# Performance work log

Measured on AMD Instinct MI355X. Metric: run time of the kernel, lower is better.

## Reference

```python
import jax, jax.numpy as jnp
import numpy as np

NUM_NODES = 65536      # 16 graphs x 4096 nodes
NODES_PER_GRAPH = 4096
NUM_GRAPHS = 16
NUM_EDGES = 1048576    # avg degree 16
DIM = 64


def setup_inputs() -> dict:
    key = jax.random.key(0)
    ks = jax.random.split(key, 10)
    # edges constrained within each component graph (batched-graph semantics)
    eper = NUM_EDGES // NUM_GRAPHS
    gid = np.repeat(np.arange(NUM_GRAPHS), eper)
    rng = np.random.default_rng(0)
    src = jnp.asarray(rng.integers(0, NODES_PER_GRAPH, NUM_EDGES) + gid * NODES_PER_GRAPH, dtype=jnp.int64)
    dst = jnp.asarray(rng.integers(0, NODES_PER_GRAPH, NUM_EDGES) + gid * NODES_PER_GRAPH, dtype=jnp.int64)
    s = 1.0 / np.sqrt(DIM)
    return {
        "x": jax.random.normal(ks[0], (NUM_NODES, DIM), dtype=jnp.float32),
        "W1": jax.random.normal(ks[1], (DIM, DIM), dtype=jnp.float32) * s,
        "b1": jnp.zeros((DIM,), dtype=jnp.float32),
        "W2": jax.random.normal(ks[2], (DIM, DIM), dtype=jnp.float32) * s,
        "b2": jnp.zeros((DIM,), dtype=jnp.float32),
        "W3": jax.random.normal(ks[3], (DIM, DIM), dtype=jnp.float32) * s,
        "b3": jnp.zeros((DIM,), dtype=jnp.float32),
        "src": src,
        "dst": dst,
        "num_graphs": NUM_GRAPHS,
    }


def _sym_norms(src, dst, n):
    ones = jnp.ones(src.shape[0], dtype=jnp.float32)
    deg_out = jax.ops.segment_sum(ones, src, num_segments=n)
    deg_in = jax.ops.segment_sum(ones, dst, num_segments=n)
    inv_sqrt = lambda d: jnp.where(d > 0, d, 1.0) ** -0.5 * (d > 0)
    return inv_sqrt(deg_out), inv_sqrt(deg_in)


def _graph_conv(x, W, b, src, dst, norm_src, norm_dst, n):
    # DGL GraphConv, norm='both': h = D_in^{-1/2} A D_out^{-1/2} (X W) + b
    h = (x * norm_src[:, None]) @ W          # [N, D]
    msg = h[src]                              # [E, D] gather
    agg = jax.ops.segment_sum(msg, dst, num_segments=n)  # [N, D] scatter-add
    return agg * norm_dst[:, None] + b


def reference(x, W1, b1, W2, b2, W3, b3, src, dst, num_graphs):
    n = x.shape[0]
    norm_src, norm_dst = _sym_norms(src, dst, n)
    h = _graph_conv(x, W1, b1, src, dst, norm_src, norm_dst, n)
    h = _graph_conv(h, W2, b2, src, dst, norm_src, norm_dst, n)
    h = _graph_conv(h, W3, b3, src, dst, norm_src, norm_dst, n)
    # unbatch + pad to max_num_nodes + stack; equal-size graphs -> pure reshape
    return h.reshape(num_graphs, n // num_graphs, h.shape[-1])
```

## Files before the change

kernel.cpp:

```cpp
#include <hip/hip_runtime.h>
#include <hip/hip_fp16.h>

#define DIM 64
#define NG  16
#define CPG 16
#define NPG 4096
#define LSTR 68
#define HISTB (NG*CPG)
#define GGN 32

__global__ __launch_bounds__(256) void k1_hist_gemm(
    const int* __restrict__ src, const int* __restrict__ dst,
    int* __restrict__ hsub, int* __restrict__ dsub, int chunk, int npg,
    const float* __restrict__ x, const float* __restrict__ W1,
    __half* __restrict__ hout, int swiz)
{
    __shared__ int smem[8192];
    const int tid = threadIdx.x;
    if ((int)blockIdx.x < HISTB) {
        int* hs = smem;
        int* hd = smem + NPG;
        const int blk = blockIdx.x;
        const int g = blk / CPG;
        const int ebase = blk * chunk;
        const int nbase = g * npg;
        for (int i = tid; i < npg; i += 256) { hs[i] = 0; hd[i] = 0; }
        __syncthreads();
        for (int e = tid; e < chunk; e += 256) {
            atomicAdd(&hs[src[ebase + e] - nbase], 1);
            atomicAdd(&hd[dst[ebase + e] - nbase], 1);
        }
        __syncthreads();
        for (int i = tid; i < npg; i += 256) {
            hsub[blk * npg + i] = hs[i];
            dsub[blk * npg + i] = hd[i];
        }
    } else {
        float* Wt = (float*)smem;
        float* xs = Wt + 64 * LSTR;
        int blk = blockIdx.x - HISTB;
        if (swiz) {
            int xg = blk & 7;
            int j = blk >> 3;
            int g = xg + ((j >> 7) << 3);
            blk = (g << 7) + (j & 127);
        }
        const int row0 = blk * 32;
        for (int i = tid; i < 64 * 64; i += 256) {
            int k = i >> 6, c = i & 63;
            Wt[c * LSTR + k] = W1[i];
        }
        for (int i = tid; i < 32 * 64; i += 256) {
            int r = i >> 6, c = i & 63;
            xs[r * LSTR + c] = x[(size_t)(row0 + r) * 64 + c];
        }
        __syncthreads();
        const int c0 = tid & 31;
        const int r0 = tid >> 5;
        float acc[4][2] = {};
#pragma unroll
        for (int k = 0; k < 64; k += 4) {
            float4 w0 = *(const float4*)&Wt[(c0     ) * LSTR + k];
            float4 w1 = *(const float4*)&Wt[(c0 + 32) * LSTR + k];
#pragma unroll
            for (int rr = 0; rr < 4; ++rr) {
                float4 xv = *(const float4*)&xs[(r0 + 8 * rr) * LSTR + k];
                acc[rr][0] += xv.x * w0.x + xv.y * w0.y + xv.z * w0.z + xv.w * w0.w;
                acc[rr][1] += xv.x * w1.x + xv.y * w1.y + xv.z * w1.z + xv.w * w1.w;
            }
        }
#pragma unroll
        for (int rr = 0; rr < 4; ++rr) {
            int row = row0 + r0 + 8 * rr;
            hout[(size_t)row * 64 + c0     ] = __float2half_rn(acc[rr][0]);
            hout[(size_t)row * 64 + c0 + 32] = __float2half_rn(acc[rr][1]);
        }
    }
}

__global__ __launch_bounds__(1024) void k2_scan(
    const int* __restrict__ hsub, int* __restrict__ dsub,
    float* __restrict__ ns, float* __restrict__ nd,
    int* __restrict__ rowptr, int epg, int npg, int N, int E)
{
    __shared__ int ddeg[NPG];
    __shared__ int wsum[16];
    const int g = blockIdx.x;
    const int t = threadIdx.x;
    const int nbase = g * npg;
    const int ebase = g * epg;
    for (int i = t; i < npg; i += 1024) {
        int sd = 0, dd = 0;
#pragma unroll
        for (int k = 0; k < CPG; ++k) {
            sd += hsub[(g * CPG + k) * npg + i];
            dd += dsub[(g * CPG + k) * npg + i];
        }
        ns[nbase + i] = sd > 0 ? rsqrtf((float)sd) : 0.0f;
        nd[nbase + i] = dd > 0 ? rsqrtf((float)dd) : 0.0f;
        ddeg[i] = dd;
    }
    __syncthreads();
    const int i0 = 4 * t;
    int d0 = ddeg[i0], d1 = ddeg[i0 + 1], d2 = ddeg[i0 + 2], d3 = ddeg[i0 + 3];
    int s4 = d0 + d1 + d2 + d3;
    const int lane = t & 63, wid = t >> 6;
    int v = s4;
#pragma unroll
    for (int off = 1; off < 64; off <<= 1) {
        int u = __shfl_up(v, off, 64);
        if (lane >= off) v += u;
    }
    if (lane == 63) wsum[wid] = v;
    __syncthreads();
    if (t < 16) {
        int w = wsum[t];
#pragma unroll
        for (int off = 1; off < 16; off <<= 1) {
            int u = __shfl_up(w, off, 16);
            if (t >= off) w += u;
        }
        wsum[t] = w;
    }
    __syncthreads();
    int incl = v + (wid > 0 ? wsum[wid - 1] : 0);
    int c = ebase + incl - s4;
    rowptr[nbase + i0    ] = c; ddeg[i0    ] = c; c += d0;
    rowptr[nbase + i0 + 1] = c; ddeg[i0 + 1] = c; c += d1;
    rowptr[nbase + i0 + 2] = c; ddeg[i0 + 2] = c; c += d2;
    rowptr[nbase + i0 + 3] = c; ddeg[i0 + 3] = c;
    if (g == 0 && t == 0) rowptr[N] = E;
    __syncthreads();
    for (int i = t; i < npg; i += 1024) {
        int cc = ddeg[i];
#pragma unroll
        for (int k = 0; k < CPG; ++k) {
            int* p = &dsub[(g * CPG + k) * npg + i];
            int old = *p; *p = cc; cc += old;
        }
    }
}

__global__ __launch_bounds__(256) void k3_fill(
    const int* __restrict__ src, const int* __restrict__ dst,
    const int* __restrict__ dsub, int* __restrict__ ssrc, int chunk, int npg)
{
    __shared__ int cur[NPG];
    const int blk = blockIdx.x;
    const int g = blk / CPG;
    const int t = threadIdx.x;
    const int ebase = blk * chunk;
    const int nbase = g * npg;
    for (int i = t; i < npg; i += 256) cur[i] = dsub[blk * npg + i];
    __syncthreads();
    for (int e = t; e < chunk; e += 256) {
        int s = src[ebase + e];
        int d = dst[ebase + e] - nbase;
        int pos = atomicAdd(&cur[d], 1);
        ssrc[pos] = s;
    }
}

__device__ __forceinline__ void acc_h4(float4& acc, uint2 u)
{
    __half2 p = *(__half2*)&u.x;
    __half2 q = *(__half2*)&u.y;
    float2 f0 = __half22float2(p);
    float2 f1 = __half22float2(q);
    acc.x += f0.x; acc.y += f0.y; acc.z += f1.x; acc.w += f1.y;
}

__device__ __forceinline__ void acc_h4s(float4& acc, uint2 u, float s)
{
    __half2 p = *(__half2*)&u.x;
    __half2 q = *(__half2*)&u.y;
    float2 f0 = __half22float2(p);
    float2 f1 = __half22float2(q);
    acc.x += s * f0.x; acc.y += s * f0.y; acc.z += s * f1.x; acc.w += s * f1.y;
}

__device__ __forceinline__ float4 gather_node(
    const __half* __restrict__ h, const int* __restrict__ ssrc,
    const float* __restrict__ ns, int beg, int end, int sub, int nsfold)
{
    float4 acc = {0.f, 0.f, 0.f, 0.f};
    int j = beg;
    if (nsfold) {
        for (; j + 7 < end; j += 8) {
            int s0 = ssrc[j+0], s1 = ssrc[j+1], s2 = ssrc[j+2], s3 = ssrc[j+3];
            int s4 = ssrc[j+4], s5 = ssrc[j+5], s6 = ssrc[j+6], s7 = ssrc[j+7];
            float n0 = ns[s0], n1 = ns[s1], n2 = ns[s2], n3 = ns[s3];
            float n4 = ns[s4], n5 = ns[s5], n6 = ns[s6], n7 = ns[s7];
            uint2 u0 = *(const uint2*)(h + (size_t)s0 * 64 + sub * 4);
            uint2 u1 = *(const uint2*)(h + (size_t)s1 * 64 + sub * 4);
            uint2 u2 = *(const uint2*)(h + (size_t)s2 * 64 + sub * 4);
            uint2 u3 = *(const uint2*)(h + (size_t)s3 * 64 + sub * 4);
            uint2 u4 = *(const uint2*)(h + (size_t)s4 * 64 + sub * 4);
            uint2 u5 = *(const uint2*)(h + (size_t)s5 * 64 + sub * 4);
            uint2 u6 = *(const uint2*)(h + (size_t)s6 * 64 + sub * 4);
            uint2 u7 = *(const uint2*)(h + (size_t)s7 * 64 + sub * 4);
            acc_h4s(acc, u0, n0); acc_h4s(acc, u1, n1);
            acc_h4s(acc, u2, n2); acc_h4s(acc, u3, n3);
            acc_h4s(acc, u4, n4); acc_h4s(acc, u5, n5);
            acc_h4s(acc, u6, n6); acc_h4s(acc, u7, n7);
        }
    } else {
        for (; j + 7 < end; j += 8) {
            int s0 = ssrc[j+0], s1 = ssrc[j+1], s2 = ssrc[j+2], s3 = ssrc[j+3];
            int s4 = ssrc[j+4], s5 = ssrc[j+5], s6 = ssrc[j+6], s7 = ssrc[j+7];
            uint2 u0 = *(const uint2*)(h + (size_t)s0 * 64 + sub * 4);
            uint2 u1 = *(const uint2*)(h + (size_t)s1 * 64 + sub * 4);
            uint2 u2 = *(const uint2*)(h + (size_t)s2 * 64 + sub * 4);
            uint2 u3 = *(const uint2*)(h + (size_t)s3 * 64 + sub * 4);
            uint2 u4 = *(const uint2*)(h + (size_t)s4 * 64 + sub * 4);
            uint2 u5 = *(const uint2*)(h + (size_t)s5 * 64 + sub * 4);
            uint2 u6 = *(const uint2*)(h + (size_t)s6 * 64 + sub * 4);
            uint2 u7 = *(const uint2*)(h + (size_t)s7 * 64 + sub * 4);
            acc_h4(acc, u0); acc_h4(acc, u1); acc_h4(acc, u2); acc_h4(acc, u3);
            acc_h4(acc, u4); acc_h4(acc, u5); acc_h4(acc, u6); acc_h4(acc, u7);
        }
    }
    int rem = end - j;
    if (rem > 0) {
#pragma unroll
        for (int q = 0; q < 4; ++q) {
            int jj = j + (q < rem ? q : rem - 1);
            int s = ssrc[jj];
            uint2 u = *(const uint2*)(h + (size_t)s * 64 + sub * 4);
            float sc = (q < rem) ? (nsfold ? ns[s] : 1.0f) : 0.0f;
            acc_h4s(acc, u, sc);
        }
    }
    if (rem > 4) {
#pragma unroll
        for (int q = 4; q < 8; ++q) {
            int jj = j + (q < rem ? q : rem - 1);
            int s = ssrc[jj];
            uint2 u = *(const uint2*)(h + (size_t)s * 64 + sub * 4);
            float sc = (q < rem) ? (nsfold ? ns[s] : 1.0f) : 0.0f;
            acc_h4s(acc, u, sc);
        }
    }
    return acc;
}

__global__ __launch_bounds__(256) void gg_kernel(
    const __half* __restrict__ h, const int* __restrict__ ssrc,
    const int* __restrict__ rowptr, const float* __restrict__ ns,
    const float* __restrict__ nd, const float* __restrict__ bprev,
    const float* __restrict__ W, __half* __restrict__ hout,
    int N, int nsfold, int swiz)
{
    __shared__ float Ws[64 * 64];
    __shared__ float us[GGN][64];
    int blk = blockIdx.x;
    if (swiz) {
        int xg = blk & 7;
        int j = blk >> 3;
        int g = xg + ((j >> 7) << 3);
        blk = (g << 7) + (j & 127);
    }
    const int tid = threadIdx.x;
    for (int i = tid; i < 64 * 64; i += 256) Ws[i] = W[i];

    const int wv = tid >> 6;
    const int lane = tid & 63;
    const int grp = lane >> 4;
    const int sub = lane & 15;

#pragma unroll
    for (int p = 0; p < GGN / 16; ++p) {
        int nl = p * 16 + wv * 4 + grp;
        int w = blk * GGN + nl;
        if (w < N) {
            int beg = rowptr[w], end = rowptr[w + 1];
            float4 acc = gather_node(h, ssrc, ns, beg, end, sub, nsfold);
            float sw = ns[w];
            float alpha = nd[w] * sw;
            float4 bv = *(const float4*)(bprev + sub * 4);
            float4 uo;
            uo.x = acc.x * alpha + sw * bv.x;
            uo.y = acc.y * alpha + sw * bv.y;
            uo.z = acc.z * alpha + sw * bv.z;
            uo.w = acc.w * alpha + sw * bv.w;
            *(float4*)&us[nl][sub * 4] = uo;
        }
    }
    __syncthreads();
    const int c = tid & 63;
#pragma unroll
    for (int m = 0; m < 8; ++m) {
        int nl = (tid >> 6) + 4 * m;
        int w = blk * GGN + nl;
        if (w >= N) continue;
        const float* ur = us[nl];
        float y = 0.f;
#pragma unroll
        for (int k = 0; k < 64; k += 4) {
            float4 uv = *(const float4*)&ur[k];
            y += uv.x * Ws[(k    ) * 64 + c]
               + uv.y * Ws[(k + 1) * 64 + c]
               + uv.z * Ws[(k + 2) * 64 + c]
               + uv.w * Ws[(k + 3) * 64 + c];
        }
        hout[(size_t)w * 64 + c] = __float2half_rn(y);
    }
}

__global__ __launch_bounds__(256) void gather_kernel(
    const __half* __restrict__ h, const int* __restrict__ ssrc,
    const int* __restrict__ rowptr, float* __restrict__ out,
    const float* __restrict__ nd, const float* __restrict__ b,
    int N, int swiz)
{
    int blk = blockIdx.x;
    if (swiz) {
        int x = blk & 7;
        int j = blk >> 3;
        int g = x + ((j >> 8) << 3);
        blk = (g << 8) + (j & 255);
    }
    const int wv = threadIdx.x >> 6;
    const int lane = threadIdx.x & 63;
    const int grp = lane >> 4;
    const int sub = lane & 15;
    int w = blk * 16 + wv * 4 + grp;
    if (w >= N) return;
    int beg = rowptr[w], end = rowptr[w + 1];
    float4 acc = gather_node(h, ssrc, (const float*)nullptr, beg, end, sub, 0);
    float n = nd[w];
    const float4 bv = *(const float4*)(b + sub * 4);
    acc.x = acc.x * n + bv.x;
    acc.y = acc.y * n + bv.y;
    acc.z = acc.z * n + bv.z;
    acc.w = acc.w * n + bv.w;
    *(float4*)(out + (size_t)w * 64 + sub * 4) = acc;
}

extern "C" void kernel_launch(void* const* d_in, const int* in_sizes, int n_in,
                              void* d_out, int out_size, void* d_ws, size_t ws_size,
                              hipStream_t stream)
{
    const float* x  = (const float*)d_in[0];
    const float* W1 = (const float*)d_in[1];
    const float* b1 = (const float*)d_in[2];
    const float* W2 = (const float*)d_in[3];
    const float* b2 = (const float*)d_in[4];
    const float* W3 = (const float*)d_in[5];
    const float* b3 = (const float*)d_in[6];
    const int*  src = (const int*)d_in[7];
    const int*  dst = (const int*)d_in[8];

    const int E = in_sizes[7];
    const int N = in_sizes[0] / DIM;
    const int epg = E / NG;
    const int npg = N / NG;
    const int chunk = epg / CPG;

    float*  ns     = (float*)d_ws;
    float*  nd     = ns + N;
    __half* hA     = (__half*)(nd + N);
    __half* hB     = hA + (size_t)N * DIM;
    int*    rowptr = (int*)(hB + (size_t)N * DIM);
    int*    ssrc   = rowptr + N + 1;
    int*    hsub   = ssrc + E;
    int*    dsub   = hsub + (size_t)HISTB * npg;
    float*  agg    = (float*)d_out;

    const int swiz = (N == 65536 && npg == 4096) ? 1 : 0;

    k1_hist_gemm<<<HISTB + N / 32, 256, 0, stream>>>(
        src, dst, hsub, dsub, chunk, npg, x, W1, hA, swiz);
    k2_scan<<<NG, 1024, 0, stream>>>(
        hsub, dsub, ns, nd, rowptr, epg, npg, N, E);
    k3_fill<<<HISTB, 256, 0, stream>>>(src, dst, dsub, ssrc, chunk, npg);

    gg_kernel<<<N / GGN, 256, 0, stream>>>(
        hA, ssrc, rowptr, ns, nd, b1, W2, hB, N, 1, swiz);
    gg_kernel<<<N / GGN, 256, 0, stream>>>(
        hB, ssrc, rowptr, ns, nd, b2, W3, hA, N, 0, swiz);
    gather_kernel<<<N / 16, 256, 0, stream>>>(
        hA, ssrc, rowptr, agg, nd, b3, N, swiz);
}
```

Baseline: 237.2 us.

## Prescale first-layer features by source norm and widen gathers to 16-byte loads

The first GEMM now writes fp32 output, and extra blocks in the CSR fill kernel scale it by the source-degree norm and convert it to fp16. This removes the per-edge ns[] lookups from the first gather layer. The gather path now uses 8 lanes per node with uint4 loads and software-pipelined index/feature prefetch, so each block handles twice as many nodes. gg_kernel drops the shared-memory copy of W, reads W from global/L1 with register blocking over 8 rows, and adds an occupancy hint to launch_bounds. The cost is an extra fp32 buffer write and read, plus higher register pressure.

```diff
diff --git a/kernel.cpp b/kernel.cpp
--- a/kernel.cpp
+++ b/kernel.cpp
@@ -8,12 +8,13 @@
 #define LSTR 68
 #define HISTB (NG*CPG)
 #define GGN 32
+#define USTR 68
 
 __global__ __launch_bounds__(256) void k1_hist_gemm(
     const int* __restrict__ src, const int* __restrict__ dst,
     int* __restrict__ hsub, int* __restrict__ dsub, int chunk, int npg,
     const float* __restrict__ x, const float* __restrict__ W1,
-    __half* __restrict__ hout, int swiz)
+    float* __restrict__ hout, int swiz)
 {
     __shared__ int smem[8192];
     const int tid = threadIdx.x;
@@ -72,8 +73,8 @@
 #pragma unroll
         for (int rr = 0; rr < 4; ++rr) {
             int row = row0 + r0 + 8 * rr;
-            hout[(size_t)row * 64 + c0     ] = __float2half_rn(acc[rr][0]);
-            hout[(size_t)row * 64 + c0 + 32] = __float2half_rn(acc[rr][1]);
+            hout[(size_t)row * 64 + c0     ] = acc[rr][0];
+            hout[(size_t)row * 64 + c0 + 32] = acc[rr][1];
         }
     }
 }
@@ -143,82 +144,113 @@
 
 __global__ __launch_bounds__(256) void k3_fill(
     const int* __restrict__ src, const int* __restrict__ dst,
-    const int* __restrict__ dsub, int* __restrict__ ssrc, int chunk, int npg)
-{
-    __shared__ int cur[NPG];
-    const int blk = blockIdx.x;
-    const int g = blk / CPG;
+    const int* __restrict__ dsub, int* __restrict__ ssrc, int chunk, int npg,
+    const float* __restrict__ hA32, const float* __restrict__ ns,
+    __half* __restrict__ hF)
+{
     const int t = threadIdx.x;
-    const int ebase = blk * chunk;
-    const int nbase = g * npg;
-    for (int i = t; i < npg; i += 256) cur[i] = dsub[blk * npg + i];
-    __syncthreads();
-    for (int e = t; e < chunk; e += 256) {
-        int s = src[ebase + e];
-        int d = dst[ebase + e] - nbase;
-        int pos = atomicAdd(&cur[d], 1);
-        ssrc[pos] = s;
-    }
-}
-
-__device__ __forceinline__ void acc_h4(float4& acc, uint2 u)
-{
-    __half2 p = *(__half2*)&u.x;
-    __half2 q = *(__half2*)&u.y;
-    float2 f0 = __half22float2(p);
-    float2 f1 = __half22float2(q);
-    acc.x += f0.x; acc.y += f0.y; acc.z += f1.x; acc.w += f1.y;
-}
-
-__device__ __forceinline__ void acc_h4s(float4& acc, uint2 u, float s)
-{
-    __half2 p = *(__half2*)&u.x;
-    __half2 q = *(__half2*)&u.y;
-    float2 f0 = __half22float2(p);
-    float2 f1 = __half22float2(q);
-    acc.x += s * f0.x; acc.y += s * f0.y; acc.z += s * f1.x; acc.w += s * f1.y;
-}
-
-__device__ __forceinline__ float4 gather_node(
+    if ((int)blockIdx.x < HISTB) {
+        __shared__ int cur[NPG];
+        const int blk = blockIdx.x;
+        const int g = blk / CPG;
+        const int ebase = blk * chunk;
+        const int nbase = g * npg;
+        for (int i = t; i < npg; i += 256) cur[i] = dsub[blk * npg + i];
+        __syncthreads();
+        for (int e = t; e < chunk; e += 256) {
+            int s = src[ebase + e];
+            int d = dst[ebase + e] - nbase;
+            int pos = atomicAdd(&cur[d], 1);
+            ssrc[pos] = s;
+        }
+    } else {
+        const int sb = blockIdx.x - HISTB;
+        const int base = sb * 16384;
+#pragma unroll
+        for (int it = 0; it < 16; ++it) {
+            int pos = base + it * 1024 + t * 4;
+            float4 v = *(const float4*)(hA32 + pos);
+            float s = ns[pos >> 6];
+            __half2 p0 = __floats2half2_rn(v.x * s, v.y * s);
+            __half2 p1 = __floats2half2_rn(v.z * s, v.w * s);
+            uint2 o;
+            o.x = *(const unsigned int*)&p0;
+            o.y = *(const unsigned int*)&p1;
+            *(uint2*)(hF + pos) = o;
+        }
+    }
+}
+
+__device__ __forceinline__ void acc_u4(float4& A, float4& B, uint4 u)
+{
+    __half2 h0 = *(__half2*)&u.x;
+    __half2 h1 = *(__half2*)&u.y;
+    __half2 h2 = *(__half2*)&u.z;
+    __half2 h3 = *(__half2*)&u.w;
+    float2 f0 = __half22float2(h0), f1 = __half22float2(h1);
+    float2 f2 = __half22float2(h2), f3 = __half22float2(h3);
+    A.x += f0.x; A.y += f0.y; A.z += f1.x; A.w += f1.y;
+    B.x += f2.x; B.y += f2.y; B.z += f3.x; B.w += f3.y;
+}
+
+__device__ __forceinline__ void acc_u4s(float4& A, float4& B, uint4 u, float s)
+{
+    __half2 h0 = *(__half2*)&u.x;
+    __half2 h1 = *(__half2*)&u.y;
+    __half2 h2 = *(__half2*)&u.z;
+    __half2 h3 = *(__half2*)&u.w;
+    float2 f0 = __half22float2(h0), f1 = __half22float2(h1);
+    float2 f2 = __half22float2(h2), f3 = __half22float2(h3);
+    A.x += s * f0.x; A.y += s * f0.y; A.z += s * f1.x; A.w += s * f1.y;
+    B.x += s * f2.x; B.y += s * f2.y; B.z += s * f3.x; B.w += s * f3.y;
+}
+
+__device__ __forceinline__ void gather_node8(
     const __half* __restrict__ h, const int* __restrict__ ssrc,
-    const float* __restrict__ ns, int beg, int end, int sub, int nsfold)
-{
-    float4 acc = {0.f, 0.f, 0.f, 0.f};
+    int beg, int end, int sub, float4& A, float4& B)
+{
+    const size_t off = (size_t)sub * 8;
     int j = beg;
-    if (nsfold) {
-        for (; j + 7 < end; j += 8) {
-            int s0 = ssrc[j+0], s1 = ssrc[j+1], s2 = ssrc[j+2], s3 = ssrc[j+3];
-            int s4 = ssrc[j+4], s5 = ssrc[j+5], s6 = ssrc[j+6], s7 = ssrc[j+7];
-            float n0 = ns[s0], n1 = ns[s1], n2 = ns[s2], n3 = ns[s3];
-            float n4 = ns[s4], n5 = ns[s5], n6 = ns[s6], n7 = ns[s7];
-            uint2 u0 = *(const uint2*)(h + (size_t)s0 * 64 + sub * 4);
-            uint2 u1 = *(const uint2*)(h + (size_t)s1 * 64 + sub * 4);
-            uint2 u2 = *(const uint2*)(h + (size_t)s2 * 64 + sub * 4);
-            uint2 u3 = *(const uint2*)(h + (size_t)s3 * 64 + sub * 4);
-            uint2 u4 = *(const uint2*)(h + (size_t)s4 * 64 + sub * 4);
-            uint2 u5 = *(const uint2*)(h + (size_t)s5 * 64 + sub * 4);
-            uint2 u6 = *(const uint2*)(h + (size_t)s6 * 64 + sub * 4);
-            uint2 u7 = *(const uint2*)(h + (size_t)s7 * 64 + sub * 4);
-            acc_h4s(acc, u0, n0); acc_h4s(acc, u1, n1);
-            acc_h4s(acc, u2, n2); acc_h4s(acc, u3, n3);
-            acc_h4s(acc, u4, n4); acc_h4s(acc, u5, n5);
-            acc_h4s(acc, u6, n6); acc_h4s(acc, u7, n7);
-        }
-    } else {
-        for (; j + 7 < end; j += 8) {
-            int s0 = ssrc[j+0], s1 = ssrc[j+1], s2 = ssrc[j+2], s3 = ssrc[j+3];
-            int s4 = ssrc[j+4], s5 = ssrc[j+5], s6 = ssrc[j+6], s7 = ssrc[j+7];
-            uint2 u0 = *(const uint2*)(h + (size_t)s0 * 64 + sub * 4);
-            uint2 u1 = *(const uint2*)(h + (size_t)s1 * 64 + sub * 4);
-            uint2 u2 = *(const uint2*)(h + (size_t)s2 * 64 + sub * 4);
-            uint2 u3 = *(const uint2*)(h + (size_t)s3 * 64 + sub * 4);
-            uint2 u4 = *(const uint2*)(h + (size_t)s4 * 64 + sub * 4);
-            uint2 u5 = *(const uint2*)(h + (size_t)s5 * 64 + sub * 4);
-            uint2 u6 = *(const uint2*)(h + (size_t)s6 * 64 + sub * 4);
-            uint2 u7 = *(const uint2*)(h + (size_t)s7 * 64 + sub * 4);
-            acc_h4(acc, u0); acc_h4(acc, u1); acc_h4(acc, u2); acc_h4(acc, u3);
-            acc_h4(acc, u4); acc_h4(acc, u5); acc_h4(acc, u6); acc_h4(acc, u7);
-        }
+    const int last = end - 8;
+    if (j <= last) {
+        int s0 = ssrc[j+0], s1 = ssrc[j+1], s2 = ssrc[j+2], s3 = ssrc[j+3];
+        int s4 = ssrc[j+4], s5 = ssrc[j+5], s6 = ssrc[j+6], s7 = ssrc[j+7];
+        uint4 a0 = *(const uint4*)(h + (size_t)s0 * 64 + off);
+        uint4 a1 = *(const uint4*)(h + (size_t)s1 * 64 + off);
+        uint4 a2 = *(const uint4*)(h + (size_t)s2 * 64 + off);
+        uint4 a3 = *(const uint4*)(h + (size_t)s3 * 64 + off);
+        uint4 a4 = *(const uint4*)(h + (size_t)s4 * 64 + off);
+        uint4 a5 = *(const uint4*)(h + (size_t)s5 * 64 + off);
+        uint4 a6 = *(const uint4*)(h + (size_t)s6 * 64 + off);
+        uint4 a7 = *(const uint4*)(h + (size_t)s7 * 64 + off);
+        j += 8;
+        bool more = (j <= last);
+        if (more) {
+            s0 = ssrc[j+0]; s1 = ssrc[j+1]; s2 = ssrc[j+2]; s3 = ssrc[j+3];
+            s4 = ssrc[j+4]; s5 = ssrc[j+5]; s6 = ssrc[j+6]; s7 = ssrc[j+7];
+        }
+        while (more) {
+            uint4 b0 = *(const uint4*)(h + (size_t)s0 * 64 + off);
+            uint4 b1 = *(const uint4*)(h + (size_t)s1 * 64 + off);
+            uint4 b2 = *(const uint4*)(h + (size_t)s2 * 64 + off);
+            uint4 b3 = *(const uint4*)(h + (size_t)s3 * 64 + off);
+            uint4 b4 = *(const uint4*)(h + (size_t)s4 * 64 + off);
+            uint4 b5 = *(const uint4*)(h + (size_t)s5 * 64 + off);
+            uint4 b6 = *(const uint4*)(h + (size_t)s6 * 64 + off);
+            uint4 b7 = *(const uint4*)(h + (size_t)s7 * 64 + off);
+            j += 8;
+            more = (j <= last);
+            if (more) {
+                s0 = ssrc[j+0]; s1 = ssrc[j+1]; s2 = ssrc[j+2]; s3 = ssrc[j+3];
+                s4 = ssrc[j+4]; s5 = ssrc[j+5]; s6 = ssrc[j+6]; s7 = ssrc[j+7];
+            }
+            acc_u4(A, B, a0); acc_u4(A, B, a1); acc_u4(A, B, a2); acc_u4(A, B, a3);
+            acc_u4(A, B, a4); acc_u4(A, B, a5); acc_u4(A, B, a6); acc_u4(A, B, a7);
+            a0 = b0; a1 = b1; a2 = b2; a3 = b3;
+            a4 = b4; a5 = b5; a6 = b6; a7 = b7;
+        }
+        acc_u4(A, B, a0); acc_u4(A, B, a1); acc_u4(A, B, a2); acc_u4(A, B, a3);
+        acc_u4(A, B, a4); acc_u4(A, B, a5); acc_u4(A, B, a6); acc_u4(A, B, a7);
     }
     int rem = end - j;
     if (rem > 0) {
@@ -226,33 +258,29 @@
         for (int q = 0; q < 4; ++q) {
             int jj = j + (q < rem ? q : rem - 1);
             int s = ssrc[jj];
-            uint2 u = *(const uint2*)(h + (size_t)s * 64 + sub * 4);
-            float sc = (q < rem) ? (nsfold ? ns[s] : 1.0f) : 0.0f;
-            acc_h4s(acc, u, sc);
-        }
-    }
-    if (rem > 4) {
-#pragma unroll
-        for (int q = 4; q < 8; ++q) {
-            int jj = j + (q < rem ? q : rem - 1);
-            int s = ssrc[jj];
-            uint2 u = *(const uint2*)(h + (size_t)s * 64 + sub * 4);
-            float sc = (q < rem) ? (nsfold ? ns[s] : 1.0f) : 0.0f;
-            acc_h4s(acc, u, sc);
-        }
-    }
-    return acc;
-}
-
-__global__ __launch_bounds__(256) void gg_kernel(
+            uint4 u = *(const uint4*)(h + (size_t)s * 64 + off);
+            acc_u4s(A, B, u, (q < rem) ? 1.0f : 0.0f);
+        }
+        if (rem > 4) {
+#pragma unroll
+            for (int q = 4; q < 8; ++q) {
+                int jj = j + (q < rem ? q : rem - 1);
+                int s = ssrc[jj];
+                uint4 u = *(const uint4*)(h + (size_t)s * 64 + off);
+                acc_u4s(A, B, u, (q < rem) ? 1.0f : 0.0f);
+            }
+        }
+    }
+}
+
+__global__ __launch_bounds__(256, 4) void gg_kernel(
     const __half* __restrict__ h, const int* __restrict__ ssrc,
     const int* __restrict__ rowptr, const float* __restrict__ ns,
     const float* __restrict__ nd, const float* __restrict__ bprev,
     const float* __restrict__ W, __half* __restrict__ hout,
-    int N, int nsfold, int swiz)
-{
-    __shared__ float Ws[64 * 64];
-    __shared__ float us[GGN][64];
+    int N, int swiz)
+{
+    __shared__ float us[GGN * USTR];
     int blk = blockIdx.x;
     if (swiz) {
         int xg = blk & 7;
@@ -261,53 +289,56 @@
         blk = (g << 7) + (j & 127);
     }
     const int tid = threadIdx.x;
-    for (int i = tid; i < 64 * 64; i += 256) Ws[i] = W[i];
-
     const int wv = tid >> 6;
     const int lane = tid & 63;
-    const int grp = lane >> 4;
-    const int sub = lane & 15;
-
-#pragma unroll
-    for (int p = 0; p < GGN / 16; ++p) {
-        int nl = p * 16 + wv * 4 + grp;
-        int w = blk * GGN + nl;
-        if (w < N) {
-            int beg = rowptr[w], end = rowptr[w + 1];
-            float4 acc = gather_node(h, ssrc, ns, beg, end, sub, nsfold);
-            float sw = ns[w];
-            float alpha = nd[w] * sw;
-            float4 bv = *(const float4*)(bprev + sub * 4);
-            float4 uo;
-            uo.x = acc.x * alpha + sw * bv.x;
-            uo.y = acc.y * alpha + sw * bv.y;
-            uo.z = acc.z * alpha + sw * bv.z;
-            uo.w = acc.w * alpha + sw * bv.w;
-            *(float4*)&us[nl][sub * 4] = uo;
-        }
+    const int grp = lane >> 3;
+    const int sub = lane & 7;
+    const int nl = wv * 8 + grp;
+    const int w = blk * GGN + nl;
+    if (w < N) {
+        int beg = rowptr[w], end = rowptr[w + 1];
+        float4 A = {0.f,0.f,0.f,0.f}, B = {0.f,0.f,0.f,0.f};
+        gather_node8(h, ssrc, beg, end, sub, A, B);
+        float sw = ns[w];
+        float alpha = nd[w] * sw;
+        float4 b0 = *(const float4*)(bprev + sub * 8);
+        float4 b1 = *(const float4*)(bprev + sub * 8 + 4);
+        A.x = A.x * alpha + sw * b0.x;
+        A.y = A.y * alpha + sw * b0.y;
+        A.z = A.z * alpha + sw * b0.z;
+        A.w = A.w * alpha + sw * b0.w;
+        B.x = B.x * alpha + sw * b1.x;
+        B.y = B.y * alpha + sw * b1.y;
+        B.z = B.z * alpha + sw * b1.z;
+        B.w = B.w * alpha + sw * b1.w;
+        *(float4*)&us[nl * USTR + sub * 8    ] = A;
+        *(float4*)&us[nl * USTR + sub * 8 + 4] = B;
     }
     __syncthreads();
     const int c = tid & 63;
+    const int nb = tid >> 6;
+    float y[8] = {0.f,0.f,0.f,0.f,0.f,0.f,0.f,0.f};
+#pragma unroll
+    for (int k = 0; k < 64; k += 4) {
+        float w0 = W[(k    ) * 64 + c];
+        float w1 = W[(k + 1) * 64 + c];
+        float w2 = W[(k + 2) * 64 + c];
+        float w3 = W[(k + 3) * 64 + c];
+#pragma unroll
+        for (int m = 0; m < 8; ++m) {
+            const float4 uv = *(const float4*)&us[(nb + 4 * m) * USTR + k];
+            y[m] += uv.x * w0 + uv.y * w1 + uv.z * w2 + uv.w * w3;
+        }
+    }
 #pragma unroll
     for (int m = 0; m < 8; ++m) {
-        int nl = (tid >> 6) + 4 * m;
-        int w = blk * GGN + nl;
-        if (w >= N) continue;
-        const float* ur = us[nl];
-        float y = 0.f;
-#pragma unroll
-        for (int k = 0; k < 64; k += 4) {
-            float4 uv = *(const float4*)&ur[k];
-            y += uv.x * Ws[(k    ) * 64 + c]
-               + uv.y * Ws[(k + 1) * 64 + c]
-               + uv.z * Ws[(k + 2) * 64 + c]
-               + uv.w * Ws[(k + 3) * 64 + c];
-        }
-        hout[(size_t)w * 64 + c] = __float2half_rn(y);
-    }
-}
-
-__global__ __launch_bounds__(256) void gather_kernel(
+        int w2i = blk * GGN + nb + 4 * m;
+        if (w2i < N)
+            hout[(size_t)w2i * 64 + c] = __float2half_rn(y[m]);
+    }
+}
+
+__global__ __launch_bounds__(256, 4) void gather_kernel(
     const __half* __restrict__ h, const int* __restrict__ ssrc,
     const int* __restrict__ rowptr, float* __restrict__ out,
     const float* __restrict__ nd, const float* __restrict__ b,
@@ -317,24 +348,27 @@
     if (swiz) {
         int x = blk & 7;
         int j = blk >> 3;
-        int g = x + ((j >> 8) << 3);
-        blk = (g << 8) + (j & 255);
+        int g = x + ((j >> 7) << 3);
+        blk = (g << 7) + (j & 127);
     }
     const int wv = threadIdx.x >> 6;
     const int lane = threadIdx.x & 63;
-    const int grp = lane >> 4;
-    const int sub = lane & 15;
-    int w = blk * 16 + wv * 4 + grp;
+    const int grp = lane >> 3;
+    const int sub = lane & 7;
+    int w = blk * 32 + wv * 8 + grp;
     if (w >= N) return;
     int beg = rowptr[w], end = rowptr[w + 1];
-    float4 acc = gather_node(h, ssrc, (const float*)nullptr, beg, end, sub, 0);
+    float4 A = {0.f,0.f,0.f,0.f}, B = {0.f,0.f,0.f,0.f};
+    gather_node8(h, ssrc, beg, end, sub, A, B);
     float n = nd[w];
-    const float4 bv = *(const float4*)(b + sub * 4);
-    acc.x = acc.x * n + bv.x;
-    acc.y = acc.y * n + bv.y;
-    acc.z = acc.z * n + bv.z;
-    acc.w = acc.w * n + bv.w;
-    *(float4*)(out + (size_t)w * 64 + sub * 4) = acc;
+    float4 b0 = *(const float4*)(b + sub * 8);
+    float4 b1 = *(const float4*)(b + sub * 8 + 4);
+    A.x = A.x * n + b0.x; A.y = A.y * n + b0.y;
+    A.z = A.z * n + b0.z; A.w = A.w * n + b0.w;
+    B.x = B.x * n + b1.x; B.y = B.y * n + b1.y;
+    B.z = B.z * n + b1.z; B.w = B.w * n + b1.w;
+    *(float4*)(out + (size_t)w * 64 + sub * 8    ) = A;
+    *(float4*)(out + (size_t)w * 64 + sub * 8 + 4) = B;
 }
 
 extern "C" void kernel_launch(void* const* d_in, const int* in_sizes, int n_in,
@@ -359,9 +393,10 @@
 
     float*  ns     = (float*)d_ws;
     float*  nd     = ns + N;
-    __half* hA     = (__half*)(nd + N);
-    __half* hB     = hA + (size_t)N * DIM;
-    int*    rowptr = (int*)(hB + (size_t)N * DIM);
+    float*  hA32   = nd + N;
+    __half* hF     = (__half*)(hA32 + (size_t)N * DIM);
+    __half* h2     = hF + (size_t)N * DIM;
+    int*    rowptr = (int*)(h2 + (size_t)N * DIM);
     int*    ssrc   = rowptr + N + 1;
     int*    hsub   = ssrc + E;
     int*    dsub   = hsub + (size_t)HISTB * npg;
@@ -370,15 +405,16 @@
     const int swiz = (N == 65536 && npg == 4096) ? 1 : 0;
 
     k1_hist_gemm<<<HISTB + N / 32, 256, 0, stream>>>(
-        src, dst, hsub, dsub, chunk, npg, x, W1, hA, swiz);
+        src, dst, hsub, dsub, chunk, npg, x, W1, hA32, swiz);
     k2_scan<<<NG, 1024, 0, stream>>>(
         hsub, dsub, ns, nd, rowptr, epg, npg, N, E);
-    k3_fill<<<HISTB, 256, 0, stream>>>(src, dst, dsub, ssrc, chunk, npg);
+    k3_fill<<<HISTB + N / 256, 256, 0, stream>>>(
+        src, dst, dsub, ssrc, chunk, npg, hA32, ns, hF);
 
     gg_kernel<<<N / GGN, 256, 0, stream>>>(
-        hA, ssrc, rowptr, ns, nd, b1, W2, hB, N, 1, swiz);
+        hF, ssrc, rowptr, ns, nd, b1, W2, h2, N, swiz);
     gg_kernel<<<N / GGN, 256, 0, stream>>>(
-        hB, ssrc, rowptr, ns, nd, b2, W3, hA, N, 0, swiz);
-    gather_kernel<<<N / 16, 256, 0, stream>>>(
-        hA, ssrc, rowptr, agg, nd, b3, N, swiz);
-}
+        h2, ssrc, rowptr, ns, nd, b2, W3, hF, N, swiz);
+    gather_kernel<<<N / 32, 256, 0, stream>>>(
+        hF, ssrc, rowptr, agg, nd, b3, N, swiz);
+}
```

Result: slower. 938.1 us (+295.4%).

## Prescale first-layer features by source norm and software-pipeline gather loads

Applied to the files above, without the earlier changes.

The first GEMM now writes fp32 output. Extra blocks added to the CSR fill kernel multiply each row by its source norm and convert it to fp16. This removes the per-edge ns[src] lookups from the first layer's gather, so a single unscaled gather path serves all layers. The gather loop is restructured to prefetch the next 8 indices and rows before accumulating the current batch, giving more memory-level parallelism. In exchange it costs an extra fp32 write and read of the features and more registers in the gather.

```diff
diff --git a/kernel.cpp b/kernel.cpp
--- a/kernel.cpp
+++ b/kernel.cpp
@@ -13,7 +13,7 @@
     const int* __restrict__ src, const int* __restrict__ dst,
     int* __restrict__ hsub, int* __restrict__ dsub, int chunk, int npg,
     const float* __restrict__ x, const float* __restrict__ W1,
-    __half* __restrict__ hout, int swiz)
+    float* __restrict__ hout, int swiz)
 {
     __shared__ int smem[8192];
     const int tid = threadIdx.x;
@@ -72,8 +72,8 @@
 #pragma unroll
         for (int rr = 0; rr < 4; ++rr) {
             int row = row0 + r0 + 8 * rr;
-            hout[(size_t)row * 64 + c0     ] = __float2half_rn(acc[rr][0]);
-            hout[(size_t)row * 64 + c0 + 32] = __float2half_rn(acc[rr][1]);
+            hout[(size_t)row * 64 + c0     ] = acc[rr][0];
+            hout[(size_t)row * 64 + c0 + 32] = acc[rr][1];
         }
     }
 }
@@ -143,21 +143,40 @@
 
 __global__ __launch_bounds__(256) void k3_fill(
     const int* __restrict__ src, const int* __restrict__ dst,
-    const int* __restrict__ dsub, int* __restrict__ ssrc, int chunk, int npg)
-{
-    __shared__ int cur[NPG];
-    const int blk = blockIdx.x;
-    const int g = blk / CPG;
+    const int* __restrict__ dsub, int* __restrict__ ssrc, int chunk, int npg,
+    const float* __restrict__ hA32, const float* __restrict__ ns,
+    __half* __restrict__ hF)
+{
     const int t = threadIdx.x;
-    const int ebase = blk * chunk;
-    const int nbase = g * npg;
-    for (int i = t; i < npg; i += 256) cur[i] = dsub[blk * npg + i];
-    __syncthreads();
-    for (int e = t; e < chunk; e += 256) {
-        int s = src[ebase + e];
-        int d = dst[ebase + e] - nbase;
-        int pos = atomicAdd(&cur[d], 1);
-        ssrc[pos] = s;
+    if ((int)blockIdx.x < HISTB) {
+        __shared__ int cur[NPG];
+        const int blk = blockIdx.x;
+        const int g = blk / CPG;
+        const int ebase = blk * chunk;
+        const int nbase = g * npg;
+        for (int i = t; i < npg; i += 256) cur[i] = dsub[blk * npg + i];
+        __syncthreads();
+        for (int e = t; e < chunk; e += 256) {
+            int s = src[ebase + e];
+            int d = dst[ebase + e] - nbase;
+            int pos = atomicAdd(&cur[d], 1);
+            ssrc[pos] = s;
+        }
+    } else {
+        const int sb = blockIdx.x - HISTB;
+        const int base = sb * 16384;
+#pragma unroll
+        for (int it = 0; it < 16; ++it) {
+            int pos = base + it * 1024 + t * 4;
+            float4 v = *(const float4*)(hA32 + pos);
+            float s = ns[pos >> 6];
+            __half2 p0 = __floats2half2_rn(v.x * s, v.y * s);
+            __half2 p1 = __floats2half2_rn(v.z * s, v.w * s);
+            uint2 o;
+            o.x = *(const unsigned int*)&p0;
+            o.y = *(const unsigned int*)&p1;
+            *(uint2*)(hF + pos) = o;
+        }
     }
 }
 
@@ -181,44 +200,51 @@
 
 __device__ __forceinline__ float4 gather_node(
     const __half* __restrict__ h, const int* __restrict__ ssrc,
-    const float* __restrict__ ns, int beg, int end, int sub, int nsfold)
-{
+    int beg, int end, int sub)
+{
+    const size_t off = (size_t)sub * 4;
     float4 acc = {0.f, 0.f, 0.f, 0.f};
     int j = beg;
-    if (nsfold) {
-        for (; j + 7 < end; j += 8) {
-            int s0 = ssrc[j+0], s1 = ssrc[j+1], s2 = ssrc[j+2], s3 = ssrc[j+3];
-            int s4 = ssrc[j+4], s5 = ssrc[j+5], s6 = ssrc[j+6], s7 = ssrc[j+7];
-            float n0 = ns[s0], n1 = ns[s1], n2 = ns[s2], n3 = ns[s3];
-            float n4 = ns[s4], n5 = ns[s5], n6 = ns[s6], n7 = ns[s7];
-            uint2 u0 = *(const uint2*)(h + (size_t)s0 * 64 + sub * 4);
-            uint2 u1 = *(const uint2*)(h + (size_t)s1 * 64 + sub * 4);
-            uint2 u2 = *(const uint2*)(h + (size_t)s2 * 64 + sub * 4);
-            uint2 u3 = *(const uint2*)(h + (size_t)s3 * 64 + sub * 4);
-            uint2 u4 = *(const uint2*)(h + (size_t)s4 * 64 + sub * 4);
-            uint2 u5 = *(const uint2*)(h + (size_t)s5 * 64 + sub * 4);
-            uint2 u6 = *(const uint2*)(h + (size_t)s6 * 64 + sub * 4);
-            uint2 u7 = *(const uint2*)(h + (size_t)s7 * 64 + sub * 4);
-            acc_h4s(acc, u0, n0); acc_h4s(acc, u1, n1);
-            acc_h4s(acc, u2, n2); acc_h4s(acc, u3, n3);
-            acc_h4s(acc, u4, n4); acc_h4s(acc, u5, n5);
-            acc_h4s(acc, u6, n6); acc_h4s(acc, u7, n7);
-        }
-    } else {
-        for (; j + 7 < end; j += 8) {
-            int s0 = ssrc[j+0], s1 = ssrc[j+1], s2 = ssrc[j+2], s3 = ssrc[j+3];
-            int s4 = ssrc[j+4], s5 = ssrc[j+5], s6 = ssrc[j+6], s7 = ssrc[j+7];
-            uint2 u0 = *(const uint2*)(h + (size_t)s0 * 64 + sub * 4);
-            uint2 u1 = *(const uint2*)(h + (size_t)s1 * 64 + sub * 4);
-            uint2 u2 = *(const uint2*)(h + (size_t)s2 * 64 + sub * 4);
-            uint2 u3 = *(const uint2*)(h + (size_t)s3 * 64 + sub * 4);
-            uint2 u4 = *(const uint2*)(h + (size_t)s4 * 64 + sub * 4);
-            uint2 u5 = *(const uint2*)(h + (size_t)s5 * 64 + sub * 4);
-            uint2 u6 = *(const uint2*)(h + (size_t)s6 * 64 + sub * 4);
-            uint2 u7 = *(const uint2*)(h + (size_t)s7 * 64 + sub * 4);
-            acc_h4(acc, u0); acc_h4(acc, u1); acc_h4(acc, u2); acc_h4(acc, u3);
-            acc_h4(acc, u4); acc_h4(acc, u5); acc_h4(acc, u6); acc_h4(acc, u7);
-        }
+    const int last = end - 8;
+    if (j <= last) {
+        int s0 = ssrc[j+0], s1 = ssrc[j+1], s2 = ssrc[j+2], s3 = ssrc[j+3];
+        int s4 = ssrc[j+4], s5 = ssrc[j+5], s6 = ssrc[j+6], s7 = ssrc[j+7];
+        uint2 a0 = *(const uint2*)(h + (size_t)s0 * 64 + off);
+        uint2 a1 = *(const uint2*)(h + (size_t)s1 * 64 + off);
+        uint2 a2 = *(const uint2*)(h + (size_t)s2 * 64 + off);
+        uint2 a3 = *(const uint2*)(h + (size_t)s3 * 64 + off);
+        uint2 a4 = *(const uint2*)(h + (size_t)s4 * 64 + off);
+        uint2 a5 = *(const uint2*)(h + (size_t)s5 * 64 + off);
+        uint2 a6 = *(const uint2*)(h + (size_t)s6 * 64 + off);
+        uint2 a7 = *(const uint2*)(h + (size_t)s7 * 64 + off);
+        j += 8;
+        bool more = (j <= last);
+        if (more) {
+            s0 = ssrc[j+0]; s1 = ssrc[j+1]; s2 = ssrc[j+2]; s3 = ssrc[j+3];
+            s4 = ssrc[j+4]; s5 = ssrc[j+5]; s6 = ssrc[j+6]; s7 = ssrc[j+7];
+        }
+        while (more) {
+            uint2 b0 = *(const uint2*)(h + (size_t)s0 * 64 + off);
+            uint2 b1 = *(const uint2*)(h + (size_t)s1 * 64 + off);
+            uint2 b2 = *(const uint2*)(h + (size_t)s2 * 64 + off);
+            uint2 b3 = *(const uint2*)(h + (size_t)s3 * 64 + off);
+            uint2 b4 = *(const uint2*)(h + (size_t)s4 * 64 + off);
+            uint2 b5 = *(const uint2*)(h + (size_t)s5 * 64 + off);
+            uint2 b6 = *(const uint2*)(h + (size_t)s6 * 64 + off);
+            uint2 b7 = *(const uint2*)(h + (size_t)s7 * 64 + off);
+            j += 8;
+            more = (j <= last);
+            if (more) {
+                s0 = ssrc[j+0]; s1 = ssrc[j+1]; s2 = ssrc[j+2]; s3 = ssrc[j+3];
+                s4 = ssrc[j+4]; s5 = ssrc[j+5]; s6 = ssrc[j+6]; s7 = ssrc[j+7];
+            }
+            acc_h4(acc, a0); acc_h4(acc, a1); acc_h4(acc, a2); acc_h4(acc, a3);
+            acc_h4(acc, a4); acc_h4(acc, a5); acc_h4(acc, a6); acc_h4(acc, a7);
+            a0 = b0; a1 = b1; a2 = b2; a3 = b3;
+            a4 = b4; a5 = b5; a6 = b6; a7 = b7;
+        }
+        acc_h4(acc, a0); acc_h4(acc, a1); acc_h4(acc, a2); acc_h4(acc, a3);
+        acc_h4(acc, a4); acc_h4(acc, a5); acc_h4(acc, a6); acc_h4(acc, a7);
     }
     int rem = end - j;
     if (rem > 0) {
@@ -226,19 +252,17 @@
         for (int q = 0; q < 4; ++q) {
             int jj = j + (q < rem ? q : rem - 1);
             int s = ssrc[jj];
-            uint2 u = *(const uint2*)(h + (size_t)s * 64 + sub * 4);
-            float sc = (q < rem) ? (nsfold ? ns[s] : 1.0f) : 0.0f;
-            acc_h4s(acc, u, sc);
-        }
-    }
-    if (rem > 4) {
-#pragma unroll
-        for (int q = 4; q < 8; ++q) {
-            int jj = j + (q < rem ? q : rem - 1);
-            int s = ssrc[jj];
-            uint2 u = *(const uint2*)(h + (size_t)s * 64 + sub * 4);
-            float sc = (q < rem) ? (nsfold ? ns[s] : 1.0f) : 0.0f;
-            acc_h4s(acc, u, sc);
+            uint2 u = *(const uint2*)(h + (size_t)s * 64 + off);
+            acc_h4s(acc, u, (q < rem) ? 1.0f : 0.0f);
+        }
+        if (rem > 4) {
+#pragma unroll
+            for (int q = 4; q < 8; ++q) {
+                int jj = j + (q < rem ? q : rem - 1);
+                int s = ssrc[jj];
+                uint2 u = *(const uint2*)(h + (size_t)s * 64 + off);
+                acc_h4s(acc, u, (q < rem) ? 1.0f : 0.0f);
+            }
         }
     }
     return acc;
@@ -249,7 +273,7 @@
     const int* __restrict__ rowptr, const float* __restrict__ ns,
     const float* __restrict__ nd, const float* __restrict__ bprev,
     const float* __restrict__ W, __half* __restrict__ hout,
-    int N, int nsfold, int swiz)
+    int N, int swiz)
 {
     __shared__ float Ws[64 * 64];
     __shared__ float us[GGN][64];
@@ -274,7 +298,7 @@
         int w = blk * GGN + nl;
         if (w < N) {
             int beg = rowptr[w], end = rowptr[w + 1];
-            float4 acc = gather_node(h, ssrc, ns, beg, end, sub, nsfold);
+            float4 acc = gather_node(h, ssrc, beg, end, sub);
             float sw = ns[w];
             float alpha = nd[w] * sw;
             float4 bv = *(const float4*)(bprev + sub * 4);
@@ -327,7 +351,7 @@
     int w = blk * 16 + wv * 4 + grp;
     if (w >= N) return;
     int beg = rowptr[w], end = rowptr[w + 1];
-    float4 acc = gather_node(h, ssrc, (const float*)nullptr, beg, end, sub, 0);
+    float4 acc = gather_node(h, ssrc, beg, end, sub);
     float n = nd[w];
     const float4 bv = *(const float4*)(b + sub * 4);
     acc.x = acc.x * n + bv.x;
@@ -359,9 +383,10 @@
 
     float*  ns     = (float*)d_ws;
     float*  nd     = ns + N;
-    __half* hA     = (__half*)(nd + N);
-    __half* hB     = hA + (size_t)N * DIM;
-    int*    rowptr = (int*)(hB + (size_t)N * DIM);
+    float*  hA32   = nd + N;
+    __half* hF     = (__half*)(hA32 + (size_t)N * DIM);
+    __half* h2     = hF + (size_t)N * DIM;
+    int*    rowptr = (int*)(h2 + (size_t)N * DIM);
     int*    ssrc   = rowptr + N + 1;
     int*    hsub   = ssrc + E;
     int*    dsub   = hsub + (size_t)HISTB * npg;
@@ -370,15 +395,16 @@
     const int swiz = (N == 65536 && npg == 4096) ? 1 : 0;
 
     k1_hist_gemm<<<HISTB + N / 32, 256, 0, stream>>>(
-        src, dst, hsub, dsub, chunk, npg, x, W1, hA, swiz);
+        src, dst, hsub, dsub, chunk, npg, x, W1, hA32, swiz);
     k2_scan<<<NG, 1024, 0, stream>>>(
         hsub, dsub, ns, nd, rowptr, epg, npg, N, E);
-    k3_fill<<<HISTB, 256, 0, stream>>>(src, dst, dsub, ssrc, chunk, npg);
+    k3_fill<<<HISTB + N / 256, 256, 0, stream>>>(
+        src, dst, dsub, ssrc, chunk, npg, hA32, ns, hF);
 
     gg_kernel<<<N / GGN, 256, 0, stream>>>(
-        hA, ssrc, rowptr, ns, nd, b1, W2, hB, N, 1, swiz);
+        hF, ssrc, rowptr, ns, nd, b1, W2, h2, N, swiz);
     gg_kernel<<<N / GGN, 256, 0, stream>>>(
-        hB, ssrc, rowptr, ns, nd, b2, W3, hA, N, 0, swiz);
+        h2, ssrc, rowptr, ns, nd, b2, W3, hF, N, swiz);
     gather_kernel<<<N / 16, 256, 0, stream>>>(
-        hA, ssrc, rowptr, agg, nd, b3, N, swiz);
-}
+        hF, ssrc, rowptr, agg, nd, b3, N, swiz);
+}
```

New measurement: 231.1 us. 2.6% less time.
